# Kernel tuning notes

Measured on AMD Instinct MI355X. Metric: run time of the kernel, lower is better.

## Reference

```python
import jax, jax.numpy as jnp
from jax import lax
import numpy as np

B, H, W, C = 16, 128, 256, 64
D = 12            # local_max_disp // stride
H_OUT, W_OUT = 1024, 2048


def setup_inputs() -> dict:
    key = jax.random.key(0)
    ks = jax.random.split(key, 8)
    feat_l = jax.random.normal(ks[0], (B, H, W, C), dtype=jnp.float32)
    feat_r = jax.random.normal(ks[1], (B, H, W, C), dtype=jnp.float32)
    def conv_w(k, shape):
        fan_in = shape[0] * shape[1] * shape[2] * shape[3]
        return jax.random.normal(k, shape, dtype=jnp.float32) / np.sqrt(fan_in)
    return {
        'feat_l': feat_l, 'feat_r': feat_r,
        'w0': conv_w(ks[2], (3, 3, 3, 1, 4)), 'b0': jnp.zeros((4,), jnp.float32),
        'w1': conv_w(ks[3], (3, 3, 3, 4, 4)), 'b1': jnp.zeros((4,), jnp.float32),
        'w2': conv_w(ks[4], (3, 3, 3, 4, 4)), 'b2': jnp.zeros((4,), jnp.float32),
        'w3': conv_w(ks[5], (3, 3, 3, 4, 4)), 'b3': jnp.zeros((4,), jnp.float32),
        'wf': conv_w(ks[6], (3, 3, 3, 4, 1)), 'bf': jnp.zeros((1,), jnp.float32),
    }


def _cost_volume(feat_l, feat_r, max_disp, stride):
    # For disparity i: cost[:, :, w, i] = sum_c |L[b,h,w,c] - R[b,h,w-i,c]| for w >= i,
    # and sum_c |L[b,h,w,c]| for w < i (which equals diff against a zero-padded shift of R).
    planes = []
    for i in range(0, max_disp, stride):
        if i == 0:
            r_shift = feat_r
        else:
            r_shift = jnp.pad(feat_r[:, :, :-i, :], ((0, 0), (0, 0), (i, 0), (0, 0)))
        planes.append(jnp.sum(jnp.abs(feat_l - r_shift), axis=-1))
    return jnp.stack(planes, axis=-1)  # [B,H,W,D]


def _conv3d(x, w, b):
    # x: [B,H,W,D,C_in], w: [3,3,3,C_in,C_out]
    y = lax.conv_general_dilated(x, w, (1, 1, 1), 'SAME',
                                 dimension_numbers=('NHWDC', 'HWDIO', 'NHWDC'))
    return y + b


def reference(feat_l, feat_r, w0, b0, w1, b1, w2, b2, w3, b3, wf, bf):
    cost = _cost_volume(feat_l, feat_r, D, 1)          # [B,H,W,D]
    x = cost[..., None]                                 # [B,H,W,D,1]
    x = jax.nn.relu(_conv3d(x, w0, b0))
    x = jax.nn.relu(_conv3d(x, w1, b1))
    x = jax.nn.relu(_conv3d(x, w2, b2))
    x = jax.nn.relu(_conv3d(x, w3, b3))
    x = _conv3d(x, wf, bf)                              # [B,H,W,D,1]
    cost = x[..., 0]                                    # [B,H,W,D]
    sm = jax.nn.softmax(-cost, axis=-1)
    disp = jnp.arange(D, dtype=jnp.float32)
    pred = jnp.sum(sm * disp, axis=-1, keepdims=True)   # [B,H,W,1]
    out = jax.image.resize(pred, (pred.shape[0], H_OUT, W_OUT, 1), method='bilinear')
    return out
```

## Files before the change

kernel.cpp:

```cpp
#include <hip/hip_runtime.h>
#include <cstddef>

#define BB   16
#define HHY  128
#define WWX  256
#define CC   64
#define DDp  12
#define HOUT 1024
#define WOUT 2048

typedef _Float16 hf;
typedef __fp16 h2 __attribute__((ext_vector_type(2)));

__device__ __forceinline__ h2 u2h(unsigned u) { return __builtin_bit_cast(h2, u); }
__device__ __forceinline__ unsigned pkrtz(float a, float b) {
  return __builtin_bit_cast(unsigned, __builtin_amdgcn_cvt_pkrtz(a, b));
}

#if defined(__has_builtin)
#if __has_builtin(__builtin_amdgcn_fdot2)
#define FDOT2(a, b, c) __builtin_amdgcn_fdot2((a), (b), (c), false)
#endif
#endif
#ifndef FDOT2
#define FDOT2(a, b, c) ((float)(a)[0] * (float)(b)[0] + (float)(a)[1] * (float)(b)[1] + (c))
#endif

__device__ __forceinline__ float adot(unsigned lu, unsigned ru, float c) {
  const h2 d = u2h(lu) - u2h(ru);
  const unsigned au = __builtin_bit_cast(unsigned, d) & 0x7FFF7FFFu;
  return FDOT2(u2h(au), u2h(0x3C003C00u), c);
}

__global__ __launch_bounds__(256) void prep_k(const float* __restrict__ w1,
                                              const float* __restrict__ w2,
                                              const float* __restrict__ w3,
                                              const float* __restrict__ wf,
                                              hf* __restrict__ o) {
  const int t = threadIdx.x;
  for (int i = t; i < 432; i += 256) {
    const int t27 = i >> 4;
    const int ci = (i >> 2) & 3;
    const int co = i & 3;
    const int dst = (t27 * 4 + co) * 4 + ci;
    o[dst]       = (hf)w1[i];
    o[432 + dst] = (hf)w2[i];
    o[864 + dst] = (hf)w3[i];
  }
  for (int i = t; i < 108; i += 256) o[1296 + i] = (hf)wf[i];
}

#define CVS 36
#define CVHALO 11
#define CVWT 64
#define CVROWS (CVWT + CVHALO + CVWT)

__global__ __launch_bounds__(256, 8) void cost_volume_k(const float* __restrict__ L,
                                                        const float* __restrict__ R,
                                                        float* __restrict__ cost) {
  __shared__ unsigned ls[CVROWS * CVS];
  const int t = threadIdx.x;
  const int wb = blockIdx.x * CVWT;
  const int h = blockIdx.y;
  const int b = blockIdx.z;
  const size_t rowbase = ((size_t)(b * HHY + h)) * WWX;
  const float* Lrow = L + rowbase * CC;
  const float* Rrow = R + rowbase * CC;

#pragma unroll
  for (int j = 0; j < 9; ++j) {
    const int fi = t + 256 * j;
    if (fi < CVROWS * 16) {
      const int row = fi >> 4;
      const int f4 = fi & 15;
      float4 v = make_float4(0.f, 0.f, 0.f, 0.f);
      if (row < CVWT + CVHALO) {
        const int gw = wb - CVHALO + row;
        if (gw >= 0) v = *(const float4*)(Rrow + (size_t)gw * CC + 4 * f4);
      } else {
        const int gw = wb + row - (CVWT + CVHALO);
        v = *(const float4*)(Lrow + (size_t)gw * CC + 4 * f4);
      }
      *(uint2*)(&ls[row * CVS + f4 * 2]) =
          make_uint2(pkrtz(v.x, v.y), pkrtz(v.z, v.w));
    }
  }
  __syncthreads();

  const int w = t & 63;
  const int dg = t >> 6;
  const int rb0 = (w + CVHALO - dg) * CVS;
  const int rb1 = (w + CVHALO - dg - 4) * CVS;
  const int rb2 = (w + CVHALO - dg - 8) * CVS;
  const int rbL = (CVWT + CVHALO + w) * CVS;

  float a0 = 0.f, a1 = 0.f, a2 = 0.f;
#pragma unroll
  for (int k = 0; k < 8; ++k) {
    const uint4 lq = *(const uint4*)(&ls[rbL + 4 * k]);
    const uint4 r0 = *(const uint4*)(&ls[rb0 + 4 * k]);
    a0 = adot(lq.x, r0.x, a0); a0 = adot(lq.y, r0.y, a0);
    a0 = adot(lq.z, r0.z, a0); a0 = adot(lq.w, r0.w, a0);
    const uint4 r1 = *(const uint4*)(&ls[rb1 + 4 * k]);
    a1 = adot(lq.x, r1.x, a1); a1 = adot(lq.y, r1.y, a1);
    a1 = adot(lq.z, r1.z, a1); a1 = adot(lq.w, r1.w, a1);
    const uint4 r2 = *(const uint4*)(&ls[rb2 + 4 * k]);
    a2 = adot(lq.x, r2.x, a2); a2 = adot(lq.y, r2.y, a2);
    a2 = adot(lq.z, r2.z, a2); a2 = adot(lq.w, r2.w, a2);
  }

  __syncthreads();
  float* lo = (float*)ls;
  lo[w * DDp + dg]     = a0;
  lo[w * DDp + dg + 4] = a1;
  lo[w * DDp + dg + 8] = a2;
  __syncthreads();
  if (t < CVWT * DDp / 4) {
    const float4 v = *(const float4*)(&lo[4 * t]);
    *(float4*)(cost + (rowbase + wb) * DDp + 4 * t) = v;
  }
}

__global__ __launch_bounds__(256) void conv0_k(const float* __restrict__ x,
                                               const float* __restrict__ wt,
                                               const float* __restrict__ bs,
                                               hf* __restrict__ y) {
  constexpr int S = 20;
  __shared__ float ls[WWX * S];
  const int t = threadIdx.x;
  const int id = blockIdx.x;
  const int h = ((id & 7) << 4) | ((id >> 3) & 15);
  const int b = id >> 7;

  float acc[DDp][4];
#pragma unroll
  for (int co = 0; co < 4; ++co) {
    const float bv = bs[co];
#pragma unroll
    for (int d = 0; d < DDp; ++d) acc[d][co] = bv;
  }

#pragma unroll
  for (int kh = 0; kh < 3; ++kh) {
    const int hh = h + kh - 1;
    if (hh < 0 || hh >= HHY) continue;

    __syncthreads();
    const float* xr = x + ((size_t)(b * HHY + hh) * WWX) * DDp;
#pragma unroll
    for (int j = 0; j < 3; ++j) {
      const int fi4 = t + 256 * j;
      const int w_ = fi4 / 3;
      const int k_ = fi4 - w_ * 3;
      *(float4*)(&ls[w_ * S + k_ * 4]) = ((const float4*)xr)[fi4];
    }
    __syncthreads();

#pragma unroll
    for (int kw = 0; kw < 3; ++kw) {
      const int ww = t + kw - 1;
      if (ww < 0 || ww >= WWX) continue;
      const float* lp = &ls[ww * S];

      const float* wp = wt + (size_t)(kh * 3 + kw) * 12;
      float wr[12];
#pragma unroll
      for (int i = 0; i < 12; ++i) wr[i] = wp[i];

      float v[DDp];
#pragma unroll
      for (int k = 0; k < 3; ++k)
        ((float4*)v)[k] = *(const float4*)(lp + 4 * k);
#pragma unroll
      for (int vo = 0; vo < DDp; ++vo)
#pragma unroll
        for (int kd = 0; kd < 3; ++kd) {
          const int d = vo + 1 - kd;
          if (d < 0 || d >= DDp) continue;
#pragma unroll
          for (int co = 0; co < 4; ++co)
            acc[d][co] += v[vo] * wr[kd * 4 + co];
        }
    }
  }

  unsigned ov[DDp * 2];
#pragma unroll
  for (int d = 0; d < DDp; ++d) {
    ov[d * 2]     = pkrtz(fmaxf(acc[d][0], 0.f), fmaxf(acc[d][1], 0.f));
    ov[d * 2 + 1] = pkrtz(fmaxf(acc[d][2], 0.f), fmaxf(acc[d][3], 0.f));
  }
  uint4* yp = (uint4*)(y + ((size_t)(b * HHY + h) * WWX + t) * (DDp * 4));
#pragma unroll
  for (int i = 0; i < 6; ++i) yp[i] = ((uint4*)ov)[i];
}

template <int COUT, bool FUSE_SM>
__global__ __launch_bounds__(256) void convh_k(const hf* __restrict__ x,
                                               const hf* __restrict__ wh,
                                               const float* __restrict__ bs,
                                               void* __restrict__ yv) {
  constexpr int DCH = DDp * 4;
  constexpr int SU  = 26;
  __shared__ unsigned lsu[WWX * SU];

  const int t = threadIdx.x;
  const int id = blockIdx.x;
  const int h = ((id & 7) << 4) | ((id >> 3) & 15);
  const int b = id >> 7;

  float acc[DDp][COUT];
#pragma unroll
  for (int co = 0; co < COUT; ++co) {
    const float bv = bs[co];
#pragma unroll
    for (int d = 0; d < DDp; ++d) acc[d][co] = bv;
  }

  const unsigned* whu = (const unsigned*)wh;

#pragma unroll
  for (int kh = 0; kh < 3; ++kh) {
    const int hh = h + kh - 1;
    if (hh < 0 || hh >= HHY) continue;

    __syncthreads();
    const uint4* xr = (const uint4*)(x + (size_t)(b * HHY + hh) * WWX * DCH);
#pragma unroll
    for (int j = 0; j < 6; ++j) {
      const int fi4 = t + 256 * j;
      const int w_ = fi4 / 6;
      const int k_ = fi4 - w_ * 6;
      const uint4 v = xr[fi4];
      unsigned* dst = &lsu[w_ * SU + k_ * 4];
      *(uint2*)(dst)     = make_uint2(v.x, v.y);
      *(uint2*)(dst + 2) = make_uint2(v.z, v.w);
    }
    __syncthreads();

#pragma unroll
    for (int kw = 0; kw < 3; ++kw) {
      const int ww = t + kw - 1;
      if (ww < 0 || ww >= WWX) continue;

      unsigned w01[3][COUT], w23[3][COUT];
      const int tap3 = (kh * 3 + kw) * 3;
#pragma unroll
      for (int kd = 0; kd < 3; ++kd)
#pragma unroll
        for (int co = 0; co < COUT; ++co) {
          const int u0 = ((tap3 + kd) * COUT + co) * 2;
          w01[kd][co] = whu[u0];
          w23[kd][co] = whu[u0 + 1];
        }

      const unsigned* lp = &lsu[ww * SU];
#pragma unroll
      for (int vo = 0; vo < DDp; ++vo) {
        const uint2 xu = *(const uint2*)(lp + vo * 2);
        const h2 x01 = u2h(xu.x), x23 = u2h(xu.y);
#pragma unroll
        for (int kd = 0; kd < 3; ++kd) {
          const int d = vo + 1 - kd;
          if (d < 0 || d >= DDp) continue;
#pragma unroll
          for (int co = 0; co < COUT; ++co)
            acc[d][co] = FDOT2(x01, u2h(w01[kd][co]),
                         FDOT2(x23, u2h(w23[kd][co]), acc[d][co]));
        }
      }
    }
  }

  if constexpr (FUSE_SM) {
    float* y = (float*)yv;
    float mn = acc[0][0];
#pragma unroll
    for (int d = 1; d < DDp; ++d) mn = fminf(mn, acc[d][0]);
    float s = 0.f, sw = 0.f;
#pragma unroll
    for (int d = 0; d < DDp; ++d) {
      const float e = __expf(mn - acc[d][0]);
      s += e;
      sw += e * (float)d;
    }
    y[(size_t)(b * HHY + h) * WWX + t] = sw / s;
  } else {
    hf* y = (hf*)yv;
    unsigned ov[DDp * 2];
#pragma unroll
    for (int d = 0; d < DDp; ++d) {
      ov[d * 2]     = pkrtz(fmaxf(acc[d][0], 0.f), fmaxf(acc[d][1 % COUT], 0.f));
      ov[d * 2 + 1] = pkrtz(fmaxf(acc[d][2 % COUT], 0.f), fmaxf(acc[d][3 % COUT], 0.f));
    }
    uint4* yp = (uint4*)(y + ((size_t)(b * HHY + h) * WWX + t) * DCH);
#pragma unroll
    for (int i = 0; i < 6; ++i) yp[i] = ((uint4*)ov)[i];
  }
}

__global__ __launch_bounds__(256) void resize4_k(const float* __restrict__ pred,
                                                 float* __restrict__ out) {
  const int idx = blockIdx.x * 256 + threadIdx.x;
  const int xg = idx & 511;
  const int y = (idx >> 9) & 1023;
  const int b = idx >> 19;

  const int parity = xg & 1;
  const int m = xg >> 1;
  const int x0 = m - 1 + parity;
  const int x0c = max(x0, 0);
  const int x1c = min(x0 + 1, WWX - 1);
  const float wx0 = (parity ? 0.0625f : 0.5625f);

  const int py = y & 7;
  const int my = y >> 3;
  const int y0 = my - 1 + (py >= 4 ? 1 : 0);
  const float wy = (py >= 4) ? 0.0625f + (py - 4) * 0.125f : 0.5625f + py * 0.125f;
  const int y0c = max(y0, 0);
  const int y1c = min(y0 + 1, HHY - 1);

  const float* pb = pred + (size_t)b * HHY * WWX;
  const float a = pb[y0c * WWX + x0c];
  const float bv = pb[y0c * WWX + x1c];
  const float c = pb[y1c * WWX + x0c];
  const float d = pb[y1c * WWX + x1c];

  const float top0 = a + (bv - a) * wx0;
  const float bot0 = c + (d - c) * wx0;
  const float dtop = (bv - a) * 0.125f;
  const float dbot = (d - c) * 0.125f;

  float4 o;
  o.x = top0 + wy * (bot0 - top0);
  o.y = (top0 + dtop) + wy * ((bot0 + dbot) - (top0 + dtop));
  o.z = (top0 + 2.f * dtop) + wy * ((bot0 + 2.f * dbot) - (top0 + 2.f * dtop));
  o.w = (top0 + 3.f * dtop) + wy * ((bot0 + 3.f * dbot) - (top0 + 3.f * dtop));

  *(float4*)(out + (size_t)idx * 4) = o;
}

extern "C" void kernel_launch(void* const* d_in, const int* in_sizes, int n_in,
                              void* d_out, int out_size, void* d_ws, size_t ws_size,
                              hipStream_t stream) {
  const float* feat_l = (const float*)d_in[0];
  const float* feat_r = (const float*)d_in[1];
  const float* w0 = (const float*)d_in[2];
  const float* b0 = (const float*)d_in[3];
  const float* w1 = (const float*)d_in[4];
  const float* b1 = (const float*)d_in[5];
  const float* w2 = (const float*)d_in[6];
  const float* b2 = (const float*)d_in[7];
  const float* w3 = (const float*)d_in[8];
  const float* b3 = (const float*)d_in[9];
  const float* wf = (const float*)d_in[10];
  const float* bf = (const float*)d_in[11];
  float* out = (float*)d_out;

  char* ws = (char*)d_ws;
  hf*    A  = (hf*)ws;
  hf*    Bf = (hf*)(ws + 50331648);
  float* C  = (float*)(ws + 100663296);
  float* P  = (float*)(ws + 125829120);
  hf*    Wh = (hf*)(ws + 127926272);

  dim3 blk(256);
  prep_k<<<dim3(1), blk, 0, stream>>>(w1, w2, w3, wf, Wh);
  cost_volume_k<<<dim3(WWX / CVWT, HHY, BB), blk, 0, stream>>>(feat_l, feat_r, C);
  conv0_k<<<dim3(HHY * BB), blk, 0, stream>>>(C, w0, b0, A);
  convh_k<4, false><<<dim3(HHY * BB), blk, 0, stream>>>(A,  Wh,        b1, Bf);
  convh_k<4, false><<<dim3(HHY * BB), blk, 0, stream>>>(Bf, Wh + 432,  b2, A);
  convh_k<4, false><<<dim3(HHY * BB), blk, 0, stream>>>(A,  Wh + 864,  b3, Bf);
  convh_k<1, true ><<<dim3(HHY * BB), blk, 0, stream>>>(Bf, Wh + 1296, bf, P);

  const int ngroups = BB * HOUT * (WOUT / 4);
  resize4_k<<<dim3(ngroups / 256), blk, 0, stream>>>(P, out);
}
```

Baseline: 295.8 us.

## Process multiple cost-volume tiles per block with register prefetch and double-buffered LDS

```diff
diff --git a/kernel.cpp b/kernel.cpp
--- a/kernel.cpp
+++ b/kernel.cpp
@@ -54,26 +54,25 @@
 #define CVHALO 11
 #define CVWT 64
 #define CVROWS (CVWT + CVHALO + CVWT)
-
-__global__ __launch_bounds__(256, 8) void cost_volume_k(const float* __restrict__ L,
-                                                        const float* __restrict__ R,
-                                                        float* __restrict__ cost) {
-  __shared__ unsigned ls[CVROWS * CVS];
-  const int t = threadIdx.x;
-  const int wb = blockIdx.x * CVWT;
-  const int h = blockIdx.y;
-  const int b = blockIdx.z;
-  const size_t rowbase = ((size_t)(b * HHY + h)) * WWX;
+#define CVTILES 8
+
+__device__ __forceinline__ void cv_issue(const float* __restrict__ L,
+                                         const float* __restrict__ R,
+                                         int tau, int t, float4* pre) {
+  const int wt = tau & 3;
+  const int hh = (tau >> 2) & (HHY - 1);
+  const int bb = tau >> 9;
+  const size_t rowbase = ((size_t)(bb * HHY + hh)) * WWX;
   const float* Lrow = L + rowbase * CC;
   const float* Rrow = R + rowbase * CC;
-
+  const int wb = wt * CVWT;
 #pragma unroll
   for (int j = 0; j < 9; ++j) {
     const int fi = t + 256 * j;
+    float4 v = make_float4(0.f, 0.f, 0.f, 0.f);
     if (fi < CVROWS * 16) {
       const int row = fi >> 4;
       const int f4 = fi & 15;
-      float4 v = make_float4(0.f, 0.f, 0.f, 0.f);
       if (row < CVWT + CVHALO) {
         const int gw = wb - CVHALO + row;
         if (gw >= 0) v = *(const float4*)(Rrow + (size_t)gw * CC + 4 * f4);
@@ -81,43 +80,77 @@
         const int gw = wb + row - (CVWT + CVHALO);
         v = *(const float4*)(Lrow + (size_t)gw * CC + 4 * f4);
       }
-      *(uint2*)(&ls[row * CVS + f4 * 2]) =
-          make_uint2(pkrtz(v.x, v.y), pkrtz(v.z, v.w));
-    }
-  }
-  __syncthreads();
-
+    }
+    pre[j] = v;
+  }
+}
+
+__global__ __launch_bounds__(256) void cost_volume_k(const float* __restrict__ L,
+                                                     const float* __restrict__ R,
+                                                     float* __restrict__ cost) {
+  __shared__ unsigned ls[2 * CVROWS * CVS];
+  const int t = threadIdx.x;
   const int w = t & 63;
   const int dg = t >> 6;
-  const int rb0 = (w + CVHALO - dg) * CVS;
-  const int rb1 = (w + CVHALO - dg - 4) * CVS;
-  const int rb2 = (w + CVHALO - dg - 8) * CVS;
-  const int rbL = (CVWT + CVHALO + w) * CVS;
-
-  float a0 = 0.f, a1 = 0.f, a2 = 0.f;
-#pragma unroll
-  for (int k = 0; k < 8; ++k) {
-    const uint4 lq = *(const uint4*)(&ls[rbL + 4 * k]);
-    const uint4 r0 = *(const uint4*)(&ls[rb0 + 4 * k]);
-    a0 = adot(lq.x, r0.x, a0); a0 = adot(lq.y, r0.y, a0);
-    a0 = adot(lq.z, r0.z, a0); a0 = adot(lq.w, r0.w, a0);
-    const uint4 r1 = *(const uint4*)(&ls[rb1 + 4 * k]);
-    a1 = adot(lq.x, r1.x, a1); a1 = adot(lq.y, r1.y, a1);
-    a1 = adot(lq.z, r1.z, a1); a1 = adot(lq.w, r1.w, a1);
-    const uint4 r2 = *(const uint4*)(&ls[rb2 + 4 * k]);
-    a2 = adot(lq.x, r2.x, a2); a2 = adot(lq.y, r2.y, a2);
-    a2 = adot(lq.z, r2.z, a2); a2 = adot(lq.w, r2.w, a2);
-  }
-
-  __syncthreads();
-  float* lo = (float*)ls;
-  lo[w * DDp + dg]     = a0;
-  lo[w * DDp + dg + 4] = a1;
-  lo[w * DDp + dg + 8] = a2;
-  __syncthreads();
-  if (t < CVWT * DDp / 4) {
-    const float4 v = *(const float4*)(&lo[4 * t]);
-    *(float4*)(cost + (rowbase + wb) * DDp + 4 * t) = v;
+
+  float4 pre[9];
+  cv_issue(L, R, blockIdx.x * CVTILES, t, pre);
+
+  for (int k = 0; k < CVTILES; ++k) {
+    const int tau = blockIdx.x * CVTILES + k;
+    unsigned* buf = &ls[(k & 1) * CVROWS * CVS];
+
+#pragma unroll
+    for (int j = 0; j < 9; ++j) {
+      const int fi = t + 256 * j;
+      if (fi < CVROWS * 16) {
+        const int row = fi >> 4;
+        const int f4 = fi & 15;
+        *(uint2*)(&buf[row * CVS + f4 * 2]) =
+            make_uint2(pkrtz(pre[j].x, pre[j].y), pkrtz(pre[j].z, pre[j].w));
+      }
+    }
+    __syncthreads();
+
+    if (k + 1 < CVTILES) cv_issue(L, R, tau + 1, t, pre);
+
+    const int rb0 = (w + CVHALO - dg) * CVS;
+    const int rb1 = rb0 - 4 * CVS;
+    const int rb2 = rb0 - 8 * CVS;
+    const int rbL = (CVWT + CVHALO + w) * CVS;
+
+    float a0 = 0.f, a1 = 0.f, a2 = 0.f;
+#pragma unroll
+    for (int kk = 0; kk < 8; ++kk) {
+      const uint4 lq = *(const uint4*)(&buf[rbL + 4 * kk]);
+      const uint4 r0 = *(const uint4*)(&buf[rb0 + 4 * kk]);
+      a0 = adot(lq.x, r0.x, a0); a0 = adot(lq.y, r0.y, a0);
+      a0 = adot(lq.z, r0.z, a0); a0 = adot(lq.w, r0.w, a0);
+      const uint4 r1 = *(const uint4*)(&buf[rb1 + 4 * kk]);
+      a1 = adot(lq.x, r1.x, a1); a1 = adot(lq.y, r1.y, a1);
+      a1 = adot(lq.z, r1.z, a1); a1 = adot(lq.w, r1.w, a1);
+      const uint4 r2 = *(const uint4*)(&buf[rb2 + 4 * kk]);
+      a2 = adot(lq.x, r2.x, a2); a2 = adot(lq.y, r2.y, a2);
+      a2 = adot(lq.z, r2.z, a2); a2 = adot(lq.w, r2.w, a2);
+    }
+
+    __syncthreads();
+    float* lo = (float*)buf;
+    lo[w * 13 + dg]     = a0;
+    lo[w * 13 + dg + 4] = a1;
+    lo[w * 13 + dg + 8] = a2;
+    __syncthreads();
+    if (t < CVWT * DDp / 4) {
+      const int wq = t / 3;
+      const int q  = t - wq * 3;
+      const float4 v = *(const float4*)(&lo[wq * 13 + 4 * q]);
+      const int wt = tau & 3;
+      const int hh = (tau >> 2) & (HHY - 1);
+      const int bb = tau >> 9;
+      const size_t rowbase = ((size_t)(bb * HHY + hh)) * WWX;
+      *(float4*)(cost + (rowbase + wt * CVWT) * DDp + 4 * t) = v;
+    }
+    __syncthreads();
   }
 }
 
@@ -366,7 +399,7 @@
 
   dim3 blk(256);
   prep_k<<<dim3(1), blk, 0, stream>>>(w1, w2, w3, wf, Wh);
-  cost_volume_k<<<dim3(WWX / CVWT, HHY, BB), blk, 0, stream>>>(feat_l, feat_r, C);
+  cost_volume_k<<<dim3(BB * HHY * (WWX / CVWT) / CVTILES), blk, 0, stream>>>(feat_l, feat_r, C);
   conv0_k<<<dim3(HHY * BB), blk, 0, stream>>>(C, w0, b0, A);
   convh_k<4, false><<<dim3(HHY * BB), blk, 0, stream>>>(A,  Wh,        b1, Bf);
   convh_k<4, false><<<dim3(HHY * BB), blk, 0, stream>>>(Bf, Wh + 432,  b2, A);
```

Result: slower. 301.8 us (+2.0%).
